# Kernel tuning notes

Measured on AMD Instinct MI355X. Metric: run time of the kernel, lower is better.

The kernel has to match this reference:

```python
import jax, jax.numpy as jnp
import numpy as np

EPS = 1e-08

def setup_inputs() -> dict:
    key = jax.random.key(0)
    k1, k2, k3 = jax.random.split(key, 3)
    shape = (4, 8, 2048, 64)  # [B, H, N, D]
    return {
        "q": jax.random.normal(k1, shape, dtype=jnp.float32),
        "k": jax.random.normal(k2, shape, dtype=jnp.float32),
        "v": jax.random.normal(k3, shape, dtype=jnp.float32),
    }

def reference(q, k, v):
    # Performer exp-kernel linear causal attention.
    d = q.shape[-1]
    data_normalizer = d ** (-0.25)
    # stabilization: q per-row max, k per-(seq,feature)-block max
    q = q - jnp.max(q, axis=-1, keepdims=True)
    k = k - jnp.max(k, axis=(-2, -1), keepdims=True)
    q = jnp.exp(data_normalizer * q) + EPS
    k = jnp.exp(data_normalizer * k) + EPS
    # denominator: q . cumsum_n(k)
    k_cumsum = jnp.cumsum(k, axis=-2) + EPS
    D_inv = 1.0 / jnp.einsum('bhnd,bhnd->bhn', q, k_cumsum)
    # causal numerator: out[n] = q[n] . cumsum_n(k[n] outer v[n])
    kv = jnp.cumsum(k[..., :, :, None] * v[..., :, None, :], axis=-3)  # [B,H,N,Dk,Dv]
    out = jnp.einsum('bhne,bhnef->bhnf', q, kv)
    return out * D_inv[..., None]
```

## Files before the change

### kernel.cpp

```cpp
#include <hip/hip_runtime.h>


#define NSEQ 2048
#define DD 64
#define CH 64
#define NC (NSEQ / CH)
#define BHN 32
#define EPSF 1e-8f
#define NRM 0.35355339059327373f
#define C1 (NRM * 1.4426950408889634f)

typedef short bf16x8 __attribute__((ext_vector_type(8)));
typedef float f32x4 __attribute__((ext_vector_type(4)));

__device__ __forceinline__ unsigned short f2bf(float f) {
  union { float f; unsigned u; } c; c.f = f;
  unsigned u = c.u + 0x7fffu + ((c.u >> 16) & 1u);
  return (unsigned short)(u >> 16);
}
__device__ __forceinline__ float bf2f(unsigned short s) {
  union { unsigned u; float f; } c; c.u = ((unsigned)s) << 16;
  return c.f;
}

__global__ __launch_bounds__(256) void k1_partial(const float* __restrict__ kg,
                                                  const float* __restrict__ vg,
                                                  float* __restrict__ ksum,
                                                  unsigned short* __restrict__ kvws) {
  __shared__ __align__(16) unsigned short Kt[DD * 72];
  __shared__ __align__(16) unsigned short Vt[DD * 72];
  const int blk = blockIdx.x;
  const int bh = blk >> 5, c = blk & 31;
  const int t = threadIdx.x;
  const size_t base = ((size_t)bh * NSEQ + (size_t)c * CH) * DD;
  const float4* k4 = (const float4*)(kg + base);
  const float4* v4 = (const float4*)(vg + base);
#pragma unroll
  for (int r = 0; r < 4; ++r) {
    int idx4 = t + 256 * r;
    int j = idx4 >> 4, e0 = (idx4 & 15) << 2;
    float4 kk = k4[idx4];
    float kv0[4] = {kk.x, kk.y, kk.z, kk.w};
    float4 vv = v4[idx4];
    float vv0[4] = {vv.x, vv.y, vv.z, vv.w};
#pragma unroll
    for (int i = 0; i < 4; ++i) {
      Kt[(e0 + i) * 72 + j] = f2bf(exp2f(kv0[i] * C1) + EPSF);
      Vt[(e0 + i) * 72 + j] = f2bf(vv0[i]);
    }
  }
  __syncthreads();
  const int wr = t >> 6, l = t & 63, lg = l >> 4, lc = l & 15;
  bf16x8 a0 = *(const bf16x8*)&Kt[(wr * 16 + lc) * 72 + lg * 8];
  bf16x8 a1 = *(const bf16x8*)&Kt[(wr * 16 + lc) * 72 + 32 + lg * 8];
  float ks = 0.f;
#pragma unroll
  for (int i = 0; i < 8; ++i) ks += bf2f((unsigned short)a0[i]) + bf2f((unsigned short)a1[i]);
  ks += __shfl_xor(ks, 16, 64);
  ks += __shfl_xor(ks, 32, 64);
  if (lg == 0) ksum[(size_t)blk * DD + wr * 16 + lc] = ks;
  f32x4 acc[4];
#pragma unroll
  for (int ft = 0; ft < 4; ++ft) { acc[ft] = (f32x4){0.f, 0.f, 0.f, 0.f}; }
#pragma unroll
  for (int ft = 0; ft < 4; ++ft) {
    bf16x8 b0 = *(const bf16x8*)&Vt[(ft * 16 + lc) * 72 + lg * 8];
    bf16x8 b1 = *(const bf16x8*)&Vt[(ft * 16 + lc) * 72 + 32 + lg * 8];
    acc[ft] = __builtin_amdgcn_mfma_f32_16x16x32_bf16(a0, b0, acc[ft], 0, 0, 0);
    acc[ft] = __builtin_amdgcn_mfma_f32_16x16x32_bf16(a1, b1, acc[ft], 0, 0, 0);
  }
  unsigned short* kvb = kvws + (size_t)blk * (DD * DD);
  const int e0 = wr * 16 + lg * 4;
#pragma unroll
  for (int ft = 0; ft < 4; ++ft) {
    short4 w;
    w.x = (short)f2bf(acc[ft][0]);
    w.y = (short)f2bf(acc[ft][1]);
    w.z = (short)f2bf(acc[ft][2]);
    w.w = (short)f2bf(acc[ft][3]);
    *(short4*)&kvb[(ft * 16 + lc) * DD + e0] = w;
  }
}

__global__ __launch_bounds__(256) void k2_scan(float* __restrict__ ksum,
                                               unsigned short* __restrict__ kvws) {
  const int blk = blockIdx.x;
  const int t = threadIdx.x;
  if (blk < 256) {
    const int bh = blk >> 3;
    const int col = (blk & 7) * 256 + t;
    unsigned* p = (unsigned*)kvws + (size_t)bh * NC * 2048 + col;
    unsigned x[NC];
#pragma unroll
    for (int c = 0; c < NC; ++c) x[c] = p[(size_t)c * 2048];
    float a0 = 0.f, a1 = 0.f;
#pragma unroll
    for (int c = 0; c < NC; ++c) {
      float x0 = bf2f((unsigned short)(x[c] & 0xffffu));
      float x1 = bf2f((unsigned short)(x[c] >> 16));
      p[(size_t)c * 2048] = (unsigned)f2bf(a0) | ((unsigned)f2bf(a1) << 16);
      a0 += x0; a1 += x1;
    }
  } else {
    const int gid = (blk - 256) * 256 + t;
    const int bh = gid >> 6, e = gid & 63;
    float* pk = ksum + (size_t)bh * NC * DD + e;
    float x[NC];
#pragma unroll
    for (int c = 0; c < NC; ++c) x[c] = pk[(size_t)c * DD];
    float run = 0.f;
#pragma unroll
    for (int c = 0; c < NC; ++c) { pk[(size_t)c * DD] = run; run += x[c]; }
  }
}

__global__ __launch_bounds__(256) void k3_out(const float* __restrict__ qg,
                                              const float* __restrict__ kg,
                                              const float* __restrict__ vg,
                                              const float* __restrict__ ksum,
                                              const unsigned short* __restrict__ kvws,
                                              float* __restrict__ out) {
  __shared__ __align__(16) unsigned short Kb[CH * 72];
  __shared__ __align__(16) unsigned short Vt[DD * 72];
  __shared__ __align__(16) unsigned short Sl[4][16 * 40];
  const int blk = blockIdx.x;
  const int t = threadIdx.x;
  const size_t base = (size_t)blk * (CH * DD);
  const float4* k4 = (const float4*)(kg + base);
  const float4* v4 = (const float4*)(vg + base);
#pragma unroll
  for (int r = 0; r < 4; ++r) {
    int idx4 = t + 256 * r;
    int j = idx4 >> 4, e0 = (idx4 & 15) << 2;
    float4 kk = k4[idx4];
    float kv0[4] = {kk.x, kk.y, kk.z, kk.w};
    short4 w;
    w.x = (short)f2bf(exp2f(kv0[0] * C1) + EPSF);
    w.y = (short)f2bf(exp2f(kv0[1] * C1) + EPSF);
    w.z = (short)f2bf(exp2f(kv0[2] * C1) + EPSF);
    w.w = (short)f2bf(exp2f(kv0[3] * C1) + EPSF);
    *(short4*)&Kb[j * 72 + e0] = w;
    float4 vv = v4[idx4];
    float vv0[4] = {vv.x, vv.y, vv.z, vv.w};
#pragma unroll
    for (int i = 0; i < 4; ++i) Vt[(e0 + i) * 72 + j] = f2bf(vv0[i]);
  }
  const int wr = t >> 6, l = t & 63, lg = l >> 4, lc = l & 15;
  float qe[2][8];
  const float* qrow = qg + base + (size_t)(wr * 16 + lc) * DD;
#pragma unroll
  for (int kt = 0; kt < 2; ++kt) {
    float4 x = *(const float4*)(qrow + kt * 32 + lg * 8);
    float4 y = *(const float4*)(qrow + kt * 32 + lg * 8 + 4);
    qe[kt][0] = x.x; qe[kt][1] = x.y; qe[kt][2] = x.z; qe[kt][3] = x.w;
    qe[kt][4] = y.x; qe[kt][5] = y.y; qe[kt][6] = y.z; qe[kt][7] = y.w;
  }
  bf16x8 qf[2];
  float dp = 0.f;
  const float* ksp = ksum + (size_t)blk * DD;
#pragma unroll
  for (int kt = 0; kt < 2; ++kt) {
    float4 s0 = *(const float4*)(ksp + kt * 32 + lg * 8);
    float4 s1 = *(const float4*)(ksp + kt * 32 + lg * 8 + 4);
    float ksv[8] = {s0.x, s0.y, s0.z, s0.w, s1.x, s1.y, s1.z, s1.w};
#pragma unroll
    for (int i = 0; i < 8; ++i) {
      float qv = exp2f(qe[kt][i] * C1) + EPSF;
      dp += qv * (ksv[i] + EPSF);
      qf[kt][i] = (short)f2bf(qv);
    }
  }
  dp += __shfl_xor(dp, 16, 64);
  dp += __shfl_xor(dp, 32, 64);
  __syncthreads();

  f32x4 o[4];
#pragma unroll
  for (int ft = 0; ft < 4; ++ft) o[ft] = (f32x4){0.f, 0.f, 0.f, 0.f};

  const unsigned short* kvb = kvws + (size_t)blk * (DD * DD);
#pragma unroll
  for (int kt = 0; kt < 2; ++kt) {
#pragma unroll
    for (int ft = 0; ft < 4; ++ft) {
      bf16x8 b = *(const bf16x8*)(kvb + (ft * 16 + lc) * DD + kt * 32 + lg * 8);
      o[ft] = __builtin_amdgcn_mfma_f32_16x16x32_bf16(qf[kt], b, o[ft], 0, 0, 0);
    }
  }

  float rs0 = 0.f, rs1 = 0.f, rs2 = 0.f, rs3 = 0.f;
  const int irow = wr * 16 + lg * 4;
  const int ng = (wr >> 1) + 1;
  for (int g = 0; g < ng; ++g) {
#pragma unroll
    for (int cc = 0; cc < 2; ++cc) {
      const int ct = 2 * g + cc;
      bf16x8 kb0 = *(const bf16x8*)&Kb[(ct * 16 + lc) * 72 + lg * 8];
      bf16x8 kb1 = *(const bf16x8*)&Kb[(ct * 16 + lc) * 72 + 32 + lg * 8];
      f32x4 s = (f32x4){0.f, 0.f, 0.f, 0.f};
      s = __builtin_amdgcn_mfma_f32_16x16x32_bf16(qf[0], kb0, s, 0, 0, 0);
      s = __builtin_amdgcn_mfma_f32_16x16x32_bf16(qf[1], kb1, s, 0, 0, 0);
      const int j = ct * 16 + lc;
      float v0 = (j <= irow + 0) ? s[0] : 0.f;
      float v1 = (j <= irow + 1) ? s[1] : 0.f;
      float v2 = (j <= irow + 2) ? s[2] : 0.f;
      float v3 = (j <= irow + 3) ? s[3] : 0.f;
      rs0 += v0; rs1 += v1; rs2 += v2; rs3 += v3;
      unsigned short* sl = &Sl[wr][0];
      sl[(lg * 4 + 0) * 40 + cc * 16 + lc] = f2bf(v0);
      sl[(lg * 4 + 1) * 40 + cc * 16 + lc] = f2bf(v1);
      sl[(lg * 4 + 2) * 40 + cc * 16 + lc] = f2bf(v2);
      sl[(lg * 4 + 3) * 40 + cc * 16 + lc] = f2bf(v3);
    }
    bf16x8 sa = *(const bf16x8*)&Sl[wr][lc * 40 + lg * 8];
#pragma unroll
    for (int ft = 0; ft < 4; ++ft) {
      bf16x8 vb = *(const bf16x8*)&Vt[(ft * 16 + lc) * 72 + g * 32 + lg * 8];
      o[ft] = __builtin_amdgcn_mfma_f32_16x16x32_bf16(sa, vb, o[ft], 0, 0, 0);
    }
  }
#pragma unroll
  for (int m = 1; m < 16; m <<= 1) {
    rs0 += __shfl_xor(rs0, m, 64);
    rs1 += __shfl_xor(rs1, m, 64);
    rs2 += __shfl_xor(rs2, m, 64);
    rs3 += __shfl_xor(rs3, m, 64);
  }
  float rsv[4] = {rs0, rs1, rs2, rs3};
  float* op = out + base;
#pragma unroll
  for (int reg = 0; reg < 4; ++reg) {
    float d = __shfl(dp, lg * 4 + reg, 64) + rsv[reg];
    float dinv = 1.0f / d;
#pragma unroll
    for (int ft = 0; ft < 4; ++ft) {
      op[(size_t)(irow + reg) * DD + ft * 16 + lc] = o[ft][reg] * dinv;
    }
  }
}

extern "C" void kernel_launch(void* const* d_in, const int* in_sizes, int n_in,
                              void* d_out, int out_size, void* d_ws, size_t ws_size,
                              hipStream_t stream) {
  const float* q = (const float*)d_in[0];
  const float* k = (const float*)d_in[1];
  const float* v = (const float*)d_in[2];
  float* out = (float*)d_out;
  float* ksum = (float*)d_ws;
  unsigned short* kvws = (unsigned short*)(ksum + (size_t)BHN * NC * DD);

  hipLaunchKernelGGL(k1_partial, dim3(BHN * NC), dim3(256), 0, stream,
                     k, v, ksum, kvws);
  hipLaunchKernelGGL(k2_scan, dim3(264), dim3(256), 0, stream, ksum, kvws);
  hipLaunchKernelGGL(k3_out, dim3(BHN * NC), dim3(256), 0, stream,
                     q, k, v, ksum, kvws, out);
}
```

Measured before the change: 108.2 us.

## Fuse three attention kernels into one cooperative kernel with grid syncs

Merges the partial-KV, scan and output kernels into a single cooperative launch of 512 blocks, each handling two chunks, with grid-wide barriers between phases. K and V are exponentiated and staged into shared memory once and reused in the output phase, so the output phase no longer reloads them from global memory. This removes two kernel launch gaps and duplicate K/V loads. In exchange it uses more shared memory per block, which may reduce occupancy, and adds two grid syncs plus a limit on grid size for cooperative residency.

```diff
diff --git a/kernel.cpp b/kernel.cpp
--- a/kernel.cpp
+++ b/kernel.cpp
@@ -1,11 +1,15 @@
 #include <hip/hip_runtime.h>
-
+#include <hip/hip_cooperative_groups.h>
+
+
+namespace cg = cooperative_groups;
 
 #define NSEQ 2048
 #define DD 64
 #define CH 64
 #define NC (NSEQ / CH)
 #define BHN 32
+#define NCHUNK (BHN * NC)
 #define EPSF 1e-8f
 #define NRM 0.35355339059327373f
 #define C1 (NRM * 1.4426950408889634f)
@@ -23,218 +27,212 @@
   return c.f;
 }
 
-__global__ __launch_bounds__(256) void k1_partial(const float* __restrict__ kg,
+__global__ __launch_bounds__(256) void perf_fused(const float* __restrict__ qg,
+                                                  const float* __restrict__ kg,
                                                   const float* __restrict__ vg,
                                                   float* __restrict__ ksum,
-                                                  unsigned short* __restrict__ kvws) {
-  __shared__ __align__(16) unsigned short Kt[DD * 72];
-  __shared__ __align__(16) unsigned short Vt[DD * 72];
-  const int blk = blockIdx.x;
-  const int bh = blk >> 5, c = blk & 31;
-  const int t = threadIdx.x;
-  const size_t base = ((size_t)bh * NSEQ + (size_t)c * CH) * DD;
-  const float4* k4 = (const float4*)(kg + base);
-  const float4* v4 = (const float4*)(vg + base);
-#pragma unroll
-  for (int r = 0; r < 4; ++r) {
-    int idx4 = t + 256 * r;
-    int j = idx4 >> 4, e0 = (idx4 & 15) << 2;
-    float4 kk = k4[idx4];
-    float kv0[4] = {kk.x, kk.y, kk.z, kk.w};
-    float4 vv = v4[idx4];
-    float vv0[4] = {vv.x, vv.y, vv.z, vv.w};
-#pragma unroll
-    for (int i = 0; i < 4; ++i) {
-      Kt[(e0 + i) * 72 + j] = f2bf(exp2f(kv0[i] * C1) + EPSF);
-      Vt[(e0 + i) * 72 + j] = f2bf(vv0[i]);
-    }
-  }
-  __syncthreads();
-  const int wr = t >> 6, l = t & 63, lg = l >> 4, lc = l & 15;
-  bf16x8 a0 = *(const bf16x8*)&Kt[(wr * 16 + lc) * 72 + lg * 8];
-  bf16x8 a1 = *(const bf16x8*)&Kt[(wr * 16 + lc) * 72 + 32 + lg * 8];
-  float ks = 0.f;
-#pragma unroll
-  for (int i = 0; i < 8; ++i) ks += bf2f((unsigned short)a0[i]) + bf2f((unsigned short)a1[i]);
-  ks += __shfl_xor(ks, 16, 64);
-  ks += __shfl_xor(ks, 32, 64);
-  if (lg == 0) ksum[(size_t)blk * DD + wr * 16 + lc] = ks;
-  f32x4 acc[4];
-#pragma unroll
-  for (int ft = 0; ft < 4; ++ft) { acc[ft] = (f32x4){0.f, 0.f, 0.f, 0.f}; }
-#pragma unroll
-  for (int ft = 0; ft < 4; ++ft) {
-    bf16x8 b0 = *(const bf16x8*)&Vt[(ft * 16 + lc) * 72 + lg * 8];
-    bf16x8 b1 = *(const bf16x8*)&Vt[(ft * 16 + lc) * 72 + 32 + lg * 8];
-    acc[ft] = __builtin_amdgcn_mfma_f32_16x16x32_bf16(a0, b0, acc[ft], 0, 0, 0);
-    acc[ft] = __builtin_amdgcn_mfma_f32_16x16x32_bf16(a1, b1, acc[ft], 0, 0, 0);
-  }
-  unsigned short* kvb = kvws + (size_t)blk * (DD * DD);
-  const int e0 = wr * 16 + lg * 4;
-#pragma unroll
-  for (int ft = 0; ft < 4; ++ft) {
-    short4 w;
-    w.x = (short)f2bf(acc[ft][0]);
-    w.y = (short)f2bf(acc[ft][1]);
-    w.z = (short)f2bf(acc[ft][2]);
-    w.w = (short)f2bf(acc[ft][3]);
-    *(short4*)&kvb[(ft * 16 + lc) * DD + e0] = w;
-  }
-}
-
-__global__ __launch_bounds__(256) void k2_scan(float* __restrict__ ksum,
-                                               unsigned short* __restrict__ kvws) {
-  const int blk = blockIdx.x;
-  const int t = threadIdx.x;
-  if (blk < 256) {
-    const int bh = blk >> 3;
-    const int col = (blk & 7) * 256 + t;
-    unsigned* p = (unsigned*)kvws + (size_t)bh * NC * 2048 + col;
-    unsigned x[NC];
-#pragma unroll
-    for (int c = 0; c < NC; ++c) x[c] = p[(size_t)c * 2048];
-    float a0 = 0.f, a1 = 0.f;
-#pragma unroll
-    for (int c = 0; c < NC; ++c) {
-      float x0 = bf2f((unsigned short)(x[c] & 0xffffu));
-      float x1 = bf2f((unsigned short)(x[c] >> 16));
-      p[(size_t)c * 2048] = (unsigned)f2bf(a0) | ((unsigned)f2bf(a1) << 16);
-      a0 += x0; a1 += x1;
-    }
-  } else {
-    const int gid = (blk - 256) * 256 + t;
-    const int bh = gid >> 6, e = gid & 63;
-    float* pk = ksum + (size_t)bh * NC * DD + e;
-    float x[NC];
-#pragma unroll
-    for (int c = 0; c < NC; ++c) x[c] = pk[(size_t)c * DD];
-    float run = 0.f;
-#pragma unroll
-    for (int c = 0; c < NC; ++c) { pk[(size_t)c * DD] = run; run += x[c]; }
-  }
-}
-
-__global__ __launch_bounds__(256) void k3_out(const float* __restrict__ qg,
-                                              const float* __restrict__ kg,
-                                              const float* __restrict__ vg,
-                                              const float* __restrict__ ksum,
-                                              const unsigned short* __restrict__ kvws,
-                                              float* __restrict__ out) {
-  __shared__ __align__(16) unsigned short Kb[CH * 72];
-  __shared__ __align__(16) unsigned short Vt[DD * 72];
+                                                  unsigned short* __restrict__ kvws,
+                                                  float* __restrict__ out) {
+  __shared__ __align__(16) unsigned short Kt[2][DD * 72];
+  __shared__ __align__(16) unsigned short Kb[2][CH * 72];
+  __shared__ __align__(16) unsigned short Vt[2][DD * 72];
   __shared__ __align__(16) unsigned short Sl[4][16 * 40];
   const int blk = blockIdx.x;
   const int t = threadIdx.x;
-  const size_t base = (size_t)blk * (CH * DD);
-  const float4* k4 = (const float4*)(kg + base);
-  const float4* v4 = (const float4*)(vg + base);
-#pragma unroll
-  for (int r = 0; r < 4; ++r) {
-    int idx4 = t + 256 * r;
-    int j = idx4 >> 4, e0 = (idx4 & 15) << 2;
-    float4 kk = k4[idx4];
-    float kv0[4] = {kk.x, kk.y, kk.z, kk.w};
-    short4 w;
-    w.x = (short)f2bf(exp2f(kv0[0] * C1) + EPSF);
-    w.y = (short)f2bf(exp2f(kv0[1] * C1) + EPSF);
-    w.z = (short)f2bf(exp2f(kv0[2] * C1) + EPSF);
-    w.w = (short)f2bf(exp2f(kv0[3] * C1) + EPSF);
-    *(short4*)&Kb[j * 72 + e0] = w;
-    float4 vv = v4[idx4];
-    float vv0[4] = {vv.x, vv.y, vv.z, vv.w};
-#pragma unroll
-    for (int i = 0; i < 4; ++i) Vt[(e0 + i) * 72 + j] = f2bf(vv0[i]);
-  }
+  const int gc0 = blk * 2;
   const int wr = t >> 6, l = t & 63, lg = l >> 4, lc = l & 15;
-  float qe[2][8];
-  const float* qrow = qg + base + (size_t)(wr * 16 + lc) * DD;
-#pragma unroll
-  for (int kt = 0; kt < 2; ++kt) {
-    float4 x = *(const float4*)(qrow + kt * 32 + lg * 8);
-    float4 y = *(const float4*)(qrow + kt * 32 + lg * 8 + 4);
-    qe[kt][0] = x.x; qe[kt][1] = x.y; qe[kt][2] = x.z; qe[kt][3] = x.w;
-    qe[kt][4] = y.x; qe[kt][5] = y.y; qe[kt][6] = y.z; qe[kt][7] = y.w;
-  }
-  bf16x8 qf[2];
-  float dp = 0.f;
-  const float* ksp = ksum + (size_t)blk * DD;
-#pragma unroll
-  for (int kt = 0; kt < 2; ++kt) {
-    float4 s0 = *(const float4*)(ksp + kt * 32 + lg * 8);
-    float4 s1 = *(const float4*)(ksp + kt * 32 + lg * 8 + 4);
-    float ksv[8] = {s0.x, s0.y, s0.z, s0.w, s1.x, s1.y, s1.z, s1.w};
-#pragma unroll
-    for (int i = 0; i < 8; ++i) {
-      float qv = exp2f(qe[kt][i] * C1) + EPSF;
-      dp += qv * (ksv[i] + EPSF);
-      qf[kt][i] = (short)f2bf(qv);
-    }
-  }
-  dp += __shfl_xor(dp, 16, 64);
-  dp += __shfl_xor(dp, 32, 64);
+
+#pragma unroll
+  for (int cc = 0; cc < 2; ++cc) {
+    const size_t base = (size_t)(gc0 + cc) * (CH * DD);
+    const float4* k4 = (const float4*)(kg + base);
+    const float4* v4 = (const float4*)(vg + base);
+#pragma unroll
+    for (int r = 0; r < 4; ++r) {
+      int idx4 = t + 256 * r;
+      int j = idx4 >> 4, e0 = (idx4 & 15) << 2;
+      float4 kk = k4[idx4];
+      float ke[4];
+      ke[0] = exp2f(kk.x * C1) + EPSF;
+      ke[1] = exp2f(kk.y * C1) + EPSF;
+      ke[2] = exp2f(kk.z * C1) + EPSF;
+      ke[3] = exp2f(kk.w * C1) + EPSF;
+      short4 w;
+      w.x = (short)f2bf(ke[0]); w.y = (short)f2bf(ke[1]);
+      w.z = (short)f2bf(ke[2]); w.w = (short)f2bf(ke[3]);
+      *(short4*)&Kb[cc][j * 72 + e0] = w;
+      float4 vv = v4[idx4];
+      float vv0[4] = {vv.x, vv.y, vv.z, vv.w};
+#pragma unroll
+      for (int i = 0; i < 4; ++i) {
+        Kt[cc][(e0 + i) * 72 + j] = f2bf(ke[i]);
+        Vt[cc][(e0 + i) * 72 + j] = f2bf(vv0[i]);
+      }
+    }
+  }
   __syncthreads();
-
-  f32x4 o[4];
-#pragma unroll
-  for (int ft = 0; ft < 4; ++ft) o[ft] = (f32x4){0.f, 0.f, 0.f, 0.f};
-
-  const unsigned short* kvb = kvws + (size_t)blk * (DD * DD);
-#pragma unroll
-  for (int kt = 0; kt < 2; ++kt) {
+#pragma unroll
+  for (int cc = 0; cc < 2; ++cc) {
+    const int gc = gc0 + cc;
+    bf16x8 a0 = *(const bf16x8*)&Kt[cc][(wr * 16 + lc) * 72 + lg * 8];
+    bf16x8 a1 = *(const bf16x8*)&Kt[cc][(wr * 16 + lc) * 72 + 32 + lg * 8];
+    float ks = 0.f;
+#pragma unroll
+    for (int i = 0; i < 8; ++i) ks += bf2f((unsigned short)a0[i]) + bf2f((unsigned short)a1[i]);
+    ks += __shfl_xor(ks, 16, 64);
+    ks += __shfl_xor(ks, 32, 64);
+    if (lg == 0) ksum[(size_t)gc * DD + wr * 16 + lc] = ks;
+    f32x4 acc[4];
+#pragma unroll
+    for (int ft = 0; ft < 4; ++ft) acc[ft] = (f32x4){0.f, 0.f, 0.f, 0.f};
 #pragma unroll
     for (int ft = 0; ft < 4; ++ft) {
-      bf16x8 b = *(const bf16x8*)(kvb + (ft * 16 + lc) * DD + kt * 32 + lg * 8);
-      o[ft] = __builtin_amdgcn_mfma_f32_16x16x32_bf16(qf[kt], b, o[ft], 0, 0, 0);
-    }
-  }
-
-  float rs0 = 0.f, rs1 = 0.f, rs2 = 0.f, rs3 = 0.f;
-  const int irow = wr * 16 + lg * 4;
-  const int ng = (wr >> 1) + 1;
-  for (int g = 0; g < ng; ++g) {
-#pragma unroll
-    for (int cc = 0; cc < 2; ++cc) {
-      const int ct = 2 * g + cc;
-      bf16x8 kb0 = *(const bf16x8*)&Kb[(ct * 16 + lc) * 72 + lg * 8];
-      bf16x8 kb1 = *(const bf16x8*)&Kb[(ct * 16 + lc) * 72 + 32 + lg * 8];
-      f32x4 s = (f32x4){0.f, 0.f, 0.f, 0.f};
-      s = __builtin_amdgcn_mfma_f32_16x16x32_bf16(qf[0], kb0, s, 0, 0, 0);
-      s = __builtin_amdgcn_mfma_f32_16x16x32_bf16(qf[1], kb1, s, 0, 0, 0);
-      const int j = ct * 16 + lc;
-      float v0 = (j <= irow + 0) ? s[0] : 0.f;
-      float v1 = (j <= irow + 1) ? s[1] : 0.f;
-      float v2 = (j <= irow + 2) ? s[2] : 0.f;
-      float v3 = (j <= irow + 3) ? s[3] : 0.f;
-      rs0 += v0; rs1 += v1; rs2 += v2; rs3 += v3;
-      unsigned short* sl = &Sl[wr][0];
-      sl[(lg * 4 + 0) * 40 + cc * 16 + lc] = f2bf(v0);
-      sl[(lg * 4 + 1) * 40 + cc * 16 + lc] = f2bf(v1);
-      sl[(lg * 4 + 2) * 40 + cc * 16 + lc] = f2bf(v2);
-      sl[(lg * 4 + 3) * 40 + cc * 16 + lc] = f2bf(v3);
-    }
-    bf16x8 sa = *(const bf16x8*)&Sl[wr][lc * 40 + lg * 8];
+      bf16x8 b0 = *(const bf16x8*)&Vt[cc][(ft * 16 + lc) * 72 + lg * 8];
+      bf16x8 b1 = *(const bf16x8*)&Vt[cc][(ft * 16 + lc) * 72 + 32 + lg * 8];
+      acc[ft] = __builtin_amdgcn_mfma_f32_16x16x32_bf16(a0, b0, acc[ft], 0, 0, 0);
+      acc[ft] = __builtin_amdgcn_mfma_f32_16x16x32_bf16(a1, b1, acc[ft], 0, 0, 0);
+    }
+    unsigned short* kvb = kvws + (size_t)gc * (DD * DD);
+    const int e0 = wr * 16 + lg * 4;
 #pragma unroll
     for (int ft = 0; ft < 4; ++ft) {
-      bf16x8 vb = *(const bf16x8*)&Vt[(ft * 16 + lc) * 72 + g * 32 + lg * 8];
-      o[ft] = __builtin_amdgcn_mfma_f32_16x16x32_bf16(sa, vb, o[ft], 0, 0, 0);
-    }
-  }
-#pragma unroll
-  for (int m = 1; m < 16; m <<= 1) {
-    rs0 += __shfl_xor(rs0, m, 64);
-    rs1 += __shfl_xor(rs1, m, 64);
-    rs2 += __shfl_xor(rs2, m, 64);
-    rs3 += __shfl_xor(rs3, m, 64);
-  }
-  float rsv[4] = {rs0, rs1, rs2, rs3};
-  float* op = out + base;
-#pragma unroll
-  for (int reg = 0; reg < 4; ++reg) {
-    float d = __shfl(dp, lg * 4 + reg, 64) + rsv[reg];
-    float dinv = 1.0f / d;
-#pragma unroll
-    for (int ft = 0; ft < 4; ++ft) {
-      op[(size_t)(irow + reg) * DD + ft * 16 + lc] = o[ft][reg] * dinv;
+      short4 w;
+      w.x = (short)f2bf(acc[ft][0]);
+      w.y = (short)f2bf(acc[ft][1]);
+      w.z = (short)f2bf(acc[ft][2]);
+      w.w = (short)f2bf(acc[ft][3]);
+      *(short4*)&kvb[(ft * 16 + lc) * DD + e0] = w;
+    }
+  }
+
+  __threadfence();
+  cg::this_grid().sync();
+
+  {
+    const int tid = blk * 256 + t;
+    if (tid < BHN * 2048) {
+      const int bh = tid >> 11, col = tid & 2047;
+      unsigned* p = (unsigned*)kvws + (size_t)bh * NC * 2048 + col;
+      unsigned x[NC];
+#pragma unroll
+      for (int c = 0; c < NC; ++c) x[c] = p[(size_t)c * 2048];
+      float a0 = 0.f, a1 = 0.f;
+#pragma unroll
+      for (int c = 0; c < NC; ++c) {
+        float x0 = bf2f((unsigned short)(x[c] & 0xffffu));
+        float x1 = bf2f((unsigned short)(x[c] >> 16));
+        p[(size_t)c * 2048] = (unsigned)f2bf(a0) | ((unsigned)f2bf(a1) << 16);
+        a0 += x0; a1 += x1;
+      }
+    } else if (tid < BHN * 2048 + BHN * DD) {
+      const int gid = tid - BHN * 2048;
+      const int bh = gid >> 6, e = gid & 63;
+      float* pk = ksum + (size_t)bh * NC * DD + e;
+      float x[NC];
+#pragma unroll
+      for (int c = 0; c < NC; ++c) x[c] = pk[(size_t)c * DD];
+      float run = 0.f;
+#pragma unroll
+      for (int c = 0; c < NC; ++c) { pk[(size_t)c * DD] = run; run += x[c]; }
+    }
+  }
+
+  __threadfence();
+  cg::this_grid().sync();
+
+#pragma unroll
+  for (int cc = 0; cc < 2; ++cc) {
+    const int gc = gc0 + cc;
+    const size_t base = (size_t)gc * (CH * DD);
+    float qe[2][8];
+    const float* qrow = qg + base + (size_t)(wr * 16 + lc) * DD;
+#pragma unroll
+    for (int kt = 0; kt < 2; ++kt) {
+      float4 x = *(const float4*)(qrow + kt * 32 + lg * 8);
+      float4 y = *(const float4*)(qrow + kt * 32 + lg * 8 + 4);
+      qe[kt][0] = x.x; qe[kt][1] = x.y; qe[kt][2] = x.z; qe[kt][3] = x.w;
+      qe[kt][4] = y.x; qe[kt][5] = y.y; qe[kt][6] = y.z; qe[kt][7] = y.w;
+    }
+    bf16x8 qf[2];
+    float dp = 0.f;
+    const float* ksp = ksum + (size_t)gc * DD;
+#pragma unroll
+    for (int kt = 0; kt < 2; ++kt) {
+      float4 s0 = *(const float4*)(ksp + kt * 32 + lg * 8);
+      float4 s1 = *(const float4*)(ksp + kt * 32 + lg * 8 + 4);
+      float ksv[8] = {s0.x, s0.y, s0.z, s0.w, s1.x, s1.y, s1.z, s1.w};
+#pragma unroll
+      for (int i = 0; i < 8; ++i) {
+        float qv = exp2f(qe[kt][i] * C1) + EPSF;
+        dp += qv * (ksv[i] + EPSF);
+        qf[kt][i] = (short)f2bf(qv);
+      }
+    }
+    dp += __shfl_xor(dp, 16, 64);
+    dp += __shfl_xor(dp, 32, 64);
+
+    f32x4 o[4];
+#pragma unroll
+    for (int ft = 0; ft < 4; ++ft) o[ft] = (f32x4){0.f, 0.f, 0.f, 0.f};
+
+    const unsigned short* kvb = kvws + (size_t)gc * (DD * DD);
+#pragma unroll
+    for (int kt = 0; kt < 2; ++kt) {
+#pragma unroll
+      for (int ft = 0; ft < 4; ++ft) {
+        bf16x8 b = *(const bf16x8*)(kvb + (ft * 16 + lc) * DD + kt * 32 + lg * 8);
+        o[ft] = __builtin_amdgcn_mfma_f32_16x16x32_bf16(qf[kt], b, o[ft], 0, 0, 0);
+      }
+    }
+
+    float rs0 = 0.f, rs1 = 0.f, rs2 = 0.f, rs3 = 0.f;
+    const int irow = wr * 16 + lg * 4;
+    const int ng = (wr >> 1) + 1;
+    for (int g = 0; g < ng; ++g) {
+#pragma unroll
+      for (int c2 = 0; c2 < 2; ++c2) {
+        const int ct = 2 * g + c2;
+        bf16x8 kb0 = *(const bf16x8*)&Kb[cc][(ct * 16 + lc) * 72 + lg * 8];
+        bf16x8 kb1 = *(const bf16x8*)&Kb[cc][(ct * 16 + lc) * 72 + 32 + lg * 8];
+        f32x4 s = (f32x4){0.f, 0.f, 0.f, 0.f};
+        s = __builtin_amdgcn_mfma_f32_16x16x32_bf16(qf[0], kb0, s, 0, 0, 0);
+        s = __builtin_amdgcn_mfma_f32_16x16x32_bf16(qf[1], kb1, s, 0, 0, 0);
+        const int j = ct * 16 + lc;
+        float v0 = (j <= irow + 0) ? s[0] : 0.f;
+        float v1 = (j <= irow + 1) ? s[1] : 0.f;
+        float v2 = (j <= irow + 2) ? s[2] : 0.f;
+        float v3 = (j <= irow + 3) ? s[3] : 0.f;
+        rs0 += v0; rs1 += v1; rs2 += v2; rs3 += v3;
+        unsigned short* sl = &Sl[wr][0];
+        sl[(lg * 4 + 0) * 40 + c2 * 16 + lc] = f2bf(v0);
+        sl[(lg * 4 + 1) * 40 + c2 * 16 + lc] = f2bf(v1);
+        sl[(lg * 4 + 2) * 40 + c2 * 16 + lc] = f2bf(v2);
+        sl[(lg * 4 + 3) * 40 + c2 * 16 + lc] = f2bf(v3);
+      }
+      bf16x8 sa = *(const bf16x8*)&Sl[wr][lc * 40 + lg * 8];
+#pragma unroll
+      for (int ft = 0; ft < 4; ++ft) {
+        bf16x8 vb = *(const bf16x8*)&Vt[cc][(ft * 16 + lc) * 72 + g * 32 + lg * 8];
+        o[ft] = __builtin_amdgcn_mfma_f32_16x16x32_bf16(sa, vb, o[ft], 0, 0, 0);
+      }
+    }
+#pragma unroll
+    for (int m = 1; m < 16; m <<= 1) {
+      rs0 += __shfl_xor(rs0, m, 64);
+      rs1 += __shfl_xor(rs1, m, 64);
+      rs2 += __shfl_xor(rs2, m, 64);
+      rs3 += __shfl_xor(rs3, m, 64);
+    }
+    float rsv[4] = {rs0, rs1, rs2, rs3};
+    float* op = out + base;
+#pragma unroll
+    for (int reg = 0; reg < 4; ++reg) {
+      float d = __shfl(dp, lg * 4 + reg, 64) + rsv[reg];
+      float dinv = 1.0f / d;
+#pragma unroll
+      for (int ft = 0; ft < 4; ++ft) {
+        op[(size_t)(irow + reg) * DD + ft * 16 + lc] = o[ft][reg] * dinv;
+      }
     }
   }
 }
@@ -247,11 +245,10 @@
   const float* v = (const float*)d_in[2];
   float* out = (float*)d_out;
   float* ksum = (float*)d_ws;
-  unsigned short* kvws = (unsigned short*)(ksum + (size_t)BHN * NC * DD);
-
-  hipLaunchKernelGGL(k1_partial, dim3(BHN * NC), dim3(256), 0, stream,
-                     k, v, ksum, kvws);
-  hipLaunchKernelGGL(k2_scan, dim3(264), dim3(256), 0, stream, ksum, kvws);
-  hipLaunchKernelGGL(k3_out, dim3(BHN * NC), dim3(256), 0, stream,
-                     q, k, v, ksum, kvws, out);
-}
+  unsigned short* kvws = (unsigned short*)(ksum + (size_t)NCHUNK * DD);
+
+  void* args[] = {(void*)&q, (void*)&k, (void*)&v,
+                  (void*)&ksum, (void*)&kvws, (void*)&out};
+  hipLaunchCooperativeKernel((const void*)perf_fused, dim3(NCHUNK / 2), dim3(256),
+                             args, 0, stream);
+}
```

Measured after the change: 340.6 us. +214.6%, slower.

## Fuse chunk prefix scan into output kernel, dropping separate scan launch

Applied to the files above, without the earlier changes.

Removes the separate scan kernel. Each output block now sums the partial KV states and k-sums of all preceding chunks directly from the workspace into shared memory before doing its local attention. This saves one kernel launch and the scan's read/write round trip. In exchange it adds redundant prefix summation: chunk c reads c partial matrices, so total reads grow quadratically with chunk count and blocks become load-imbalanced.

```diff
diff --git a/kernel.cpp b/kernel.cpp
--- a/kernel.cpp
+++ b/kernel.cpp
@@ -6,6 +6,7 @@
 #define CH 64
 #define NC (NSEQ / CH)
 #define BHN 32
+#define NCHUNK (BHN * NC)
 #define EPSF 1e-8f
 #define NRM 0.35355339059327373f
 #define C1 (NRM * 1.4426950408889634f)
@@ -23,16 +24,15 @@
   return c.f;
 }
 
-__global__ __launch_bounds__(256) void k1_partial(const float* __restrict__ kg,
+__global__ __launch_bounds__(256) void kA_partial(const float* __restrict__ kg,
                                                   const float* __restrict__ vg,
                                                   float* __restrict__ ksum,
                                                   unsigned short* __restrict__ kvws) {
   __shared__ __align__(16) unsigned short Kt[DD * 72];
   __shared__ __align__(16) unsigned short Vt[DD * 72];
   const int blk = blockIdx.x;
-  const int bh = blk >> 5, c = blk & 31;
   const int t = threadIdx.x;
-  const size_t base = ((size_t)bh * NSEQ + (size_t)c * CH) * DD;
+  const size_t base = (size_t)blk * (CH * DD);
   const float4* k4 = (const float4*)(kg + base);
   const float4* v4 = (const float4*)(vg + base);
 #pragma unroll
@@ -61,7 +61,7 @@
   if (lg == 0) ksum[(size_t)blk * DD + wr * 16 + lc] = ks;
   f32x4 acc[4];
 #pragma unroll
-  for (int ft = 0; ft < 4; ++ft) { acc[ft] = (f32x4){0.f, 0.f, 0.f, 0.f}; }
+  for (int ft = 0; ft < 4; ++ft) acc[ft] = (f32x4){0.f, 0.f, 0.f, 0.f};
 #pragma unroll
   for (int ft = 0; ft < 4; ++ft) {
     bf16x8 b0 = *(const bf16x8*)&Vt[(ft * 16 + lc) * 72 + lg * 8];
@@ -82,39 +82,7 @@
   }
 }
 
-__global__ __launch_bounds__(256) void k2_scan(float* __restrict__ ksum,
-                                               unsigned short* __restrict__ kvws) {
-  const int blk = blockIdx.x;
-  const int t = threadIdx.x;
-  if (blk < 256) {
-    const int bh = blk >> 3;
-    const int col = (blk & 7) * 256 + t;
-    unsigned* p = (unsigned*)kvws + (size_t)bh * NC * 2048 + col;
-    unsigned x[NC];
-#pragma unroll
-    for (int c = 0; c < NC; ++c) x[c] = p[(size_t)c * 2048];
-    float a0 = 0.f, a1 = 0.f;
-#pragma unroll
-    for (int c = 0; c < NC; ++c) {
-      float x0 = bf2f((unsigned short)(x[c] & 0xffffu));
-      float x1 = bf2f((unsigned short)(x[c] >> 16));
-      p[(size_t)c * 2048] = (unsigned)f2bf(a0) | ((unsigned)f2bf(a1) << 16);
-      a0 += x0; a1 += x1;
-    }
-  } else {
-    const int gid = (blk - 256) * 256 + t;
-    const int bh = gid >> 6, e = gid & 63;
-    float* pk = ksum + (size_t)bh * NC * DD + e;
-    float x[NC];
-#pragma unroll
-    for (int c = 0; c < NC; ++c) x[c] = pk[(size_t)c * DD];
-    float run = 0.f;
-#pragma unroll
-    for (int c = 0; c < NC; ++c) { pk[(size_t)c * DD] = run; run += x[c]; }
-  }
-}
-
-__global__ __launch_bounds__(256) void k3_out(const float* __restrict__ qg,
+__global__ __launch_bounds__(256) void kB_out(const float* __restrict__ qg,
                                               const float* __restrict__ kg,
                                               const float* __restrict__ vg,
                                               const float* __restrict__ ksum,
@@ -122,8 +90,11 @@
                                               float* __restrict__ out) {
   __shared__ __align__(16) unsigned short Kb[CH * 72];
   __shared__ __align__(16) unsigned short Vt[DD * 72];
+  __shared__ __align__(16) unsigned short KVp[DD * 72];
   __shared__ __align__(16) unsigned short Sl[4][16 * 40];
+  __shared__ float kspf[DD];
   const int blk = blockIdx.x;
+  const int bh = blk >> 5, c = blk & 31;
   const int t = threadIdx.x;
   const size_t base = (size_t)blk * (CH * DD);
   const float4* k4 = (const float4*)(kg + base);
@@ -133,17 +104,47 @@
     int idx4 = t + 256 * r;
     int j = idx4 >> 4, e0 = (idx4 & 15) << 2;
     float4 kk = k4[idx4];
-    float kv0[4] = {kk.x, kk.y, kk.z, kk.w};
     short4 w;
-    w.x = (short)f2bf(exp2f(kv0[0] * C1) + EPSF);
-    w.y = (short)f2bf(exp2f(kv0[1] * C1) + EPSF);
-    w.z = (short)f2bf(exp2f(kv0[2] * C1) + EPSF);
-    w.w = (short)f2bf(exp2f(kv0[3] * C1) + EPSF);
+    w.x = (short)f2bf(exp2f(kk.x * C1) + EPSF);
+    w.y = (short)f2bf(exp2f(kk.y * C1) + EPSF);
+    w.z = (short)f2bf(exp2f(kk.z * C1) + EPSF);
+    w.w = (short)f2bf(exp2f(kk.w * C1) + EPSF);
     *(short4*)&Kb[j * 72 + e0] = w;
     float4 vv = v4[idx4];
     float vv0[4] = {vv.x, vv.y, vv.z, vv.w};
 #pragma unroll
     for (int i = 0; i < 4; ++i) Vt[(e0 + i) * 72 + j] = f2bf(vv0[i]);
+  }
+  {
+    float pf[16];
+#pragma unroll
+    for (int i = 0; i < 16; ++i) pf[i] = 0.f;
+    const unsigned short* kvbase =
+        kvws + ((size_t)bh * NC) * (DD * DD) + (size_t)t * 16;
+    for (int j = 0; j < c; ++j) {
+      bf16x8 x0 = *(const bf16x8*)(kvbase + (size_t)j * (DD * DD));
+      bf16x8 x1 = *(const bf16x8*)(kvbase + (size_t)j * (DD * DD) + 8);
+#pragma unroll
+      for (int i = 0; i < 8; ++i) {
+        pf[i]     += bf2f((unsigned short)x0[i]);
+        pf[8 + i] += bf2f((unsigned short)x1[i]);
+      }
+    }
+    bf16x8 w0, w1;
+#pragma unroll
+    for (int i = 0; i < 8; ++i) {
+      w0[i] = (short)f2bf(pf[i]);
+      w1[i] = (short)f2bf(pf[8 + i]);
+    }
+    unsigned short* kvrow = &KVp[(t >> 2) * 72 + (t & 3) * 16];
+    *(bf16x8*)kvrow = w0;
+    *(bf16x8*)(kvrow + 8) = w1;
+  }
+  if (t < DD) {
+    float s = 0.f;
+    const float* kp = ksum + ((size_t)bh * NC) * DD + t;
+    for (int j = 0; j < c; ++j) s += kp[(size_t)j * DD];
+    kspf[t] = s;
   }
   const int wr = t >> 6, l = t & 63, lg = l >> 4, lc = l & 15;
   float qe[2][8];
@@ -155,13 +156,14 @@
     qe[kt][0] = x.x; qe[kt][1] = x.y; qe[kt][2] = x.z; qe[kt][3] = x.w;
     qe[kt][4] = y.x; qe[kt][5] = y.y; qe[kt][6] = y.z; qe[kt][7] = y.w;
   }
+  __syncthreads();
+
   bf16x8 qf[2];
   float dp = 0.f;
-  const float* ksp = ksum + (size_t)blk * DD;
 #pragma unroll
   for (int kt = 0; kt < 2; ++kt) {
-    float4 s0 = *(const float4*)(ksp + kt * 32 + lg * 8);
-    float4 s1 = *(const float4*)(ksp + kt * 32 + lg * 8 + 4);
+    float4 s0 = *(const float4*)(kspf + kt * 32 + lg * 8);
+    float4 s1 = *(const float4*)(kspf + kt * 32 + lg * 8 + 4);
     float ksv[8] = {s0.x, s0.y, s0.z, s0.w, s1.x, s1.y, s1.z, s1.w};
 #pragma unroll
     for (int i = 0; i < 8; ++i) {
@@ -172,18 +174,16 @@
   }
   dp += __shfl_xor(dp, 16, 64);
   dp += __shfl_xor(dp, 32, 64);
-  __syncthreads();
 
   f32x4 o[4];
 #pragma unroll
   for (int ft = 0; ft < 4; ++ft) o[ft] = (f32x4){0.f, 0.f, 0.f, 0.f};
 
-  const unsigned short* kvb = kvws + (size_t)blk * (DD * DD);
 #pragma unroll
   for (int kt = 0; kt < 2; ++kt) {
 #pragma unroll
     for (int ft = 0; ft < 4; ++ft) {
-      bf16x8 b = *(const bf16x8*)(kvb + (ft * 16 + lc) * DD + kt * 32 + lg * 8);
+      bf16x8 b = *(const bf16x8*)&KVp[(ft * 16 + lc) * 72 + kt * 32 + lg * 8];
       o[ft] = __builtin_amdgcn_mfma_f32_16x16x32_bf16(qf[kt], b, o[ft], 0, 0, 0);
     }
   }
@@ -193,8 +193,8 @@
   const int ng = (wr >> 1) + 1;
   for (int g = 0; g < ng; ++g) {
 #pragma unroll
-    for (int cc = 0; cc < 2; ++cc) {
-      const int ct = 2 * g + cc;
+    for (int c2 = 0; c2 < 2; ++c2) {
+      const int ct = 2 * g + c2;
       bf16x8 kb0 = *(const bf16x8*)&Kb[(ct * 16 + lc) * 72 + lg * 8];
       bf16x8 kb1 = *(const bf16x8*)&Kb[(ct * 16 + lc) * 72 + 32 + lg * 8];
       f32x4 s = (f32x4){0.f, 0.f, 0.f, 0.f};
@@ -207,10 +207,10 @@
       float v3 = (j <= irow + 3) ? s[3] : 0.f;
       rs0 += v0; rs1 += v1; rs2 += v2; rs3 += v3;
       unsigned short* sl = &Sl[wr][0];
-      sl[(lg * 4 + 0) * 40 + cc * 16 + lc] = f2bf(v0);
-      sl[(lg * 4 + 1) * 40 + cc * 16 + lc] = f2bf(v1);
-      sl[(lg * 4 + 2) * 40 + cc * 16 + lc] = f2bf(v2);
-      sl[(lg * 4 + 3) * 40 + cc * 16 + lc] = f2bf(v3);
+      sl[(lg * 4 + 0) * 40 + c2 * 16 + lc] = f2bf(v0);
+      sl[(lg * 4 + 1) * 40 + c2 * 16 + lc] = f2bf(v1);
+      sl[(lg * 4 + 2) * 40 + c2 * 16 + lc] = f2bf(v2);
+      sl[(lg * 4 + 3) * 40 + c2 * 16 + lc] = f2bf(v3);
     }
     bf16x8 sa = *(const bf16x8*)&Sl[wr][lc * 40 + lg * 8];
 #pragma unroll
@@ -247,11 +247,10 @@
   const float* v = (const float*)d_in[2];
   float* out = (float*)d_out;
   float* ksum = (float*)d_ws;
-  unsigned short* kvws = (unsigned short*)(ksum + (size_t)BHN * NC * DD);
-
-  hipLaunchKernelGGL(k1_partial, dim3(BHN * NC), dim3(256), 0, stream,
+  unsigned short* kvws = (unsigned short*)(ksum + (size_t)NCHUNK * DD);
+
+  hipLaunchKernelGGL(kA_partial, dim3(NCHUNK), dim3(256), 0, stream,
                      k, v, ksum, kvws);
-  hipLaunchKernelGGL(k2_scan, dim3(264), dim3(256), 0, stream, ksum, kvws);
-  hipLaunchKernelGGL(k3_out, dim3(BHN * NC), dim3(256), 0, stream,
+  hipLaunchKernelGGL(kB_out, dim3(NCHUNK), dim3(256), 0, stream,
                      q, k, v, ksum, kvws, out);
 }
```

After: 116.8 us. +7.9%, slower.
